# Kernel tuning notes

Measured on AMD Instinct MI355X. Metric: run time of the kernel, lower is better.

The kernel has to match this reference:

```python
import jax, jax.numpy as jnp
import numpy as np

N_NODES = 10000
N_EDGES = 160000
N_TYPES = 128          # rows in SymbolicEmbeddingsVQ table
N_SYMBOLS = 64
PATTERN_LEN = 8
SYMBOL_DIM = 16
HIDDEN = PATTERN_LEN * SYMBOL_DIM  # mode='concat' -> 128
NUM_RADIAL = 6


def setup_inputs() -> dict:
    key = jax.random.key(0)
    ks = jax.random.split(key, 10)
    x = jax.random.randint(ks[0], (N_NODES,), 0, N_TYPES)
    rbf = jax.random.normal(ks[1], (N_EDGES, NUM_RADIAL), dtype=jnp.float32)
    i = jax.random.randint(ks[2], (N_EDGES,), 0, N_NODES)
    j = jax.random.randint(ks[3], (N_EDGES,), 0, N_NODES)
    # VQ symbolic embedding params: each of 128 types is a pattern of
    # PATTERN_LEN symbol ids; symbols are vectors from a codebook.
    code_idx = jax.random.randint(ks[4], (N_TYPES, PATTERN_LEN), 0, N_SYMBOLS)
    codebook = jax.random.normal(ks[5], (N_SYMBOLS, SYMBOL_DIM), dtype=jnp.float32)
    # Linear layers (PyTorch Linear default uniform init approximated by scaled normals)
    W_rbf = jax.random.normal(ks[6], (NUM_RADIAL, HIDDEN), dtype=jnp.float32) / np.sqrt(NUM_RADIAL)
    b_rbf = jnp.zeros((HIDDEN,), dtype=jnp.float32)
    W = jax.random.normal(ks[7], (3 * HIDDEN, HIDDEN), dtype=jnp.float32) / np.sqrt(3 * HIDDEN)
    b = jnp.zeros((HIDDEN,), dtype=jnp.float32)
    return {"x": x, "rbf": rbf, "i": i, "j": j, "code_idx": code_idx,
            "codebook": codebook, "W_rbf": W_rbf, "b_rbf": b_rbf, "W": W, "b": b}


def reference(x, rbf, i, j, code_idx, codebook, W_rbf, b_rbf, W, b):
    act = jax.nn.silu
    # Symbolic VQ embedding, mode='concat': table[t] = concat of PATTERN_LEN codebook vectors
    table = codebook[code_idx].reshape(N_TYPES, HIDDEN)   # [128, hidden]
    h = table[x]                                          # [N_nodes, hidden]
    r = act(rbf @ W_rbf + b_rbf)                          # [E, hidden]
    feat = jnp.concatenate([h[i], h[j], r], axis=-1)      # [E, 3*hidden]
    return act(feat @ W + b)                              # [E, hidden]
```

## Files before the change

### kernel.cpp

```cpp
#include <hip/hip_runtime.h>
#include <hip/hip_bf16.h>
#include <stdint.h>

typedef __attribute__((ext_vector_type(8))) short bf16x8;
typedef __attribute__((ext_vector_type(4))) float f32x4;

__device__ __forceinline__ float silu_f(float x) {
    return x * __builtin_amdgcn_rcpf(1.0f + __expf(-x));
}

__device__ __forceinline__ unsigned short f2bf(float x) {
    union { float f; unsigned int u; } v; v.f = x;
    unsigned int r = v.u + 0x7fffu + ((v.u >> 16) & 1u);
    return (unsigned short)(r >> 16);
}
__device__ __forceinline__ float bf2f(unsigned short u) {
    union { unsigned int u; float f; } v; v.u = ((unsigned int)u) << 16;
    return v.f;
}

__device__ __forceinline__ void async16(void* l, const void* g) {
    auto lds3 = (__attribute__((address_space(3))) unsigned int*)(uintptr_t)l;
    auto g1   = (const __attribute__((address_space(1))) unsigned int*)(uintptr_t)g;
    __builtin_amdgcn_global_load_lds(g1, lds3, 16, 0, 0);
}

__global__ void prep_P(const int* __restrict__ code_idx,
                       const float* __restrict__ codebook,
                       const float* __restrict__ W,
                       const float* __restrict__ b,
                       unsigned short* __restrict__ P1,
                       unsigned short* __restrict__ P2,
                       unsigned short* __restrict__ Wt3)
{
    __shared__ float trow[128];
    const int t = blockIdx.x, tid = threadIdx.x;
    if (tid < 128) {
        int sym = code_idx[t * 8 + (tid >> 4)];
        trow[tid] = codebook[sym * 16 + (tid & 15)];
    } else {
        int k = tid - 128;
        Wt3[t * 128 + k] = f2bf(W[(256 + k) * 128 + t]);
    }
    __syncthreads();
    const int which = tid >> 7, o = tid & 127;
    const float* Wb = W + which * 16384;
    float acc = which ? 0.0f : b[o];
#pragma unroll 8
    for (int k = 0; k < 128; ++k)
        acc += trow[k] * Wb[k * 128 + o];
    (which ? P2 : P1)[t * 128 + o] = f2bf(acc);
}

__global__ __launch_bounds__(256, 3) void fused_main(
    const int* __restrict__ x,
    const float* __restrict__ rbf,
    const int* __restrict__ ei,
    const int* __restrict__ ej,
    const float* __restrict__ W_rbf,
    const float* __restrict__ b_rbf,
    const unsigned short* __restrict__ P1,
    const unsigned short* __restrict__ P2,
    const unsigned short* __restrict__ Wt3,
    float* __restrict__ out)
{
    __shared__ __align__(16) unsigned char lB[32768];
    __shared__ __align__(16) unsigned char lA[16384];
    __shared__ __align__(16) unsigned char lR[1536];

    const int tid  = threadIdx.x;
    const int lane = tid & 63;
    const int w    = tid >> 6;
    const int e0   = blockIdx.x * 64;

    const int quad = lane >> 4, l15 = lane & 15;
    const int wm = (w >> 1) * 32, wn = (w & 1) * 64;

    {
        const int ri = lane >> 4, ch = lane & 15;
#pragma unroll
        for (int rr = 0; rr < 8; ++rr) {
            int g = w * 8 + rr;
            int o = g * 4 + ri;
            int j = ch ^ (o & 7);
            async16(lB + g * 1024, Wt3 + o * 128 + j * 8);
        }
    }
    if (w == 0)
        async16(lR, (const unsigned char*)rbf + (size_t)e0 * 24 + lane * 16);
    else if (w == 1 && lane < 32)
        async16(lR + 1024, (const unsigned char*)rbf + (size_t)e0 * 24 + 1024 + lane * 16);

    int ti[8], tj[8];
#pragma unroll
    for (int mi = 0; mi < 2; ++mi)
#pragma unroll
        for (int r = 0; r < 4; ++r) {
            int m = wm + mi * 16 + quad * 4 + r;
            int e = e0 + m;
            ti[mi * 4 + r] = x[ei[e]];
            tj[mi * 4 + r] = x[ej[e]];
        }

    const int j16 = tid & 15, gg = tid >> 4, cb = j16 * 8;
    float wr[6][8], br[8];
#pragma unroll
    for (int q = 0; q < 6; ++q) {
        const float4* p = (const float4*)(W_rbf + q * 128 + cb);
        float4 a = p[0], c = p[1];
        wr[q][0]=a.x; wr[q][1]=a.y; wr[q][2]=a.z; wr[q][3]=a.w;
        wr[q][4]=c.x; wr[q][5]=c.y; wr[q][6]=c.z; wr[q][7]=c.w;
    }
    {
        const float4* p = (const float4*)(b_rbf + cb);
        float4 a = p[0], c = p[1];
        br[0]=a.x; br[1]=a.y; br[2]=a.z; br[3]=a.w;
        br[4]=c.x; br[5]=c.y; br[6]=c.z; br[7]=c.w;
    }

    __syncthreads();

#pragma unroll
    for (int i = 0; i < 4; ++i) {
        int m = gg * 4 + i;
        const float* rr_ = (const float*)(lR + m * 24);
        float f0 = rr_[0], f1 = rr_[1], f2 = rr_[2],
              f3 = rr_[3], f4 = rr_[4], f5 = rr_[5];
        bf16x8 pk;
#pragma unroll
        for (int c = 0; c < 8; ++c) {
            float a = br[c] + f0*wr[0][c] + f1*wr[1][c] + f2*wr[2][c]
                            + f3*wr[3][c] + f4*wr[4][c] + f5*wr[5][c];
            pk[c] = (short)f2bf(silu_f(a));
        }
        int p = j16 ^ (m & 7);
        *(bf16x8*)(lA + m * 256 + p * 16) = pk;
    }

    __syncthreads();

    unsigned short q1[2][4][4], q2[2][4][4];
#pragma unroll
    for (int mi = 0; mi < 2; ++mi)
#pragma unroll
        for (int r = 0; r < 4; ++r) {
            const unsigned short* p1r = P1 + ti[mi * 4 + r] * 128;
            const unsigned short* p2r = P2 + tj[mi * 4 + r] * 128;
#pragma unroll
            for (int ni = 0; ni < 4; ++ni) {
                int o = wn + ni * 16 + l15;
                q1[mi][r][ni] = p1r[o];
                q2[mi][r][ni] = p2r[o];
            }
        }

    f32x4 acc[2][4] = {};
    const int l7 = l15 & 7;
#pragma unroll
    for (int ks = 0; ks < 4; ++ks) {
        const int j = ks * 4 + quad;
        const int p = j ^ l7;
        bf16x8 af[2], bfv[4];
#pragma unroll
        for (int mi = 0; mi < 2; ++mi)
            af[mi] = *(const bf16x8*)(lA + (wm + mi * 16 + l15) * 256 + p * 16);
#pragma unroll
        for (int ni = 0; ni < 4; ++ni)
            bfv[ni] = *(const bf16x8*)(lB + (wn + ni * 16 + l15) * 256 + p * 16);
#pragma unroll
        for (int mi = 0; mi < 2; ++mi)
#pragma unroll
            for (int ni = 0; ni < 4; ++ni)
                acc[mi][ni] = __builtin_amdgcn_mfma_f32_16x16x32_bf16(
                    af[mi], bfv[ni], acc[mi][ni], 0, 0, 0);
    }

#pragma unroll
    for (int mi = 0; mi < 2; ++mi)
#pragma unroll
        for (int r = 0; r < 4; ++r) {
            int m = wm + mi * 16 + quad * 4 + r;
            size_t e = e0 + m;
#pragma unroll
            for (int ni = 0; ni < 4; ++ni) {
                int o = wn + ni * 16 + l15;
                float v = acc[mi][ni][r] + bf2f(q1[mi][r][ni]) + bf2f(q2[mi][r][ni]);
                out[e * 128 + o] = silu_f(v);
            }
        }
}

extern "C" void kernel_launch(void* const* d_in, const int* in_sizes, int n_in,
                              void* d_out, int out_size, void* d_ws, size_t ws_size,
                              hipStream_t stream) {
    const int*   x        = (const int*)d_in[0];
    const float* rbf      = (const float*)d_in[1];
    const int*   ei       = (const int*)d_in[2];
    const int*   ej       = (const int*)d_in[3];
    const int*   code_idx = (const int*)d_in[4];
    const float* codebook = (const float*)d_in[5];
    const float* W_rbf    = (const float*)d_in[6];
    const float* b_rbf    = (const float*)d_in[7];
    const float* W        = (const float*)d_in[8];
    const float* b        = (const float*)d_in[9];
    float* out = (float*)d_out;

    const int nE = in_sizes[2];

    if (ws_size < 98304) return;
    unsigned short* P1  = (unsigned short*)d_ws;
    unsigned short* P2  = P1 + 16384;
    unsigned short* Wt3 = P2 + 16384;

    prep_P<<<128, 256, 0, stream>>>(code_idx, codebook, W, b, P1, P2, Wt3);
    fused_main<<<nE / 64, 256, 0, stream>>>(x, rbf, ei, ej, W_rbf, b_rbf,
                                            P1, P2, Wt3, out);
}
```

Measured before the change: 132.9 us.

## Make fused kernel persistent with atomic tile queue and double-buffered prefetch

```diff
diff --git a/kernel.cpp b/kernel.cpp
--- a/kernel.cpp
+++ b/kernel.cpp
@@ -3,6 +3,7 @@
 #include <stdint.h>
 
 typedef __attribute__((ext_vector_type(8))) short bf16x8;
+typedef __attribute__((ext_vector_type(4))) short bf16x4;
 typedef __attribute__((ext_vector_type(4))) float f32x4;
 
 __device__ __forceinline__ float silu_f(float x) {
@@ -31,10 +32,12 @@
                        const float* __restrict__ b,
                        unsigned short* __restrict__ P1,
                        unsigned short* __restrict__ P2,
-                       unsigned short* __restrict__ Wt3)
+                       unsigned short* __restrict__ Wt3,
+                       int* __restrict__ counter)
 {
     __shared__ float trow[128];
     const int t = blockIdx.x, tid = threadIdx.x;
+    if (t == 0 && tid == 0) counter[0] = 0;
     if (tid < 128) {
         int sym = code_idx[t * 8 + (tid >> 4)];
         trow[tid] = codebook[sym * 16 + (tid & 15)];
@@ -62,19 +65,22 @@
     const unsigned short* __restrict__ P1,
     const unsigned short* __restrict__ P2,
     const unsigned short* __restrict__ Wt3,
-    float* __restrict__ out)
+    float* __restrict__ out,
+    int* __restrict__ counter,
+    int ntiles)
 {
     __shared__ __align__(16) unsigned char lB[32768];
     __shared__ __align__(16) unsigned char lA[16384];
-    __shared__ __align__(16) unsigned char lR[1536];
+    __shared__ __align__(16) unsigned char lR[2][1536];
+    __shared__ int lTi[2][64], lTj[2][64];
+    __shared__ int lT[2];
 
     const int tid  = threadIdx.x;
     const int lane = tid & 63;
     const int w    = tid >> 6;
-    const int e0   = blockIdx.x * 64;
-
-    const int quad = lane >> 4, l15 = lane & 15;
+    const int quad = lane >> 4, l15 = lane & 15, l7 = lane & 7;
     const int wm = (w >> 1) * 32, wn = (w & 1) * 64;
+    const unsigned char* rbfB = (const unsigned char*)rbf;
 
     {
         const int ri = lane >> 4, ch = lane & 15;
@@ -86,108 +92,131 @@
             async16(lB + g * 1024, Wt3 + o * 128 + j * 8);
         }
     }
+    const int j32 = tid & 31, grp = tid >> 5;
+    const int cb4 = j32 * 4;
+    float wr[6][4], br[4];
+#pragma unroll
+    for (int q = 0; q < 6; ++q) {
+        float4 a = *(const float4*)(W_rbf + q * 128 + cb4);
+        wr[q][0] = a.x; wr[q][1] = a.y; wr[q][2] = a.z; wr[q][3] = a.w;
+    }
+    {
+        float4 a = *(const float4*)(b_rbf + cb4);
+        br[0] = a.x; br[1] = a.y; br[2] = a.z; br[3] = a.w;
+    }
+
+    if (tid == 0) lT[0] = atomicAdd(counter, 1);
+    __syncthreads();
+    int t = lT[0];
+    if (t >= ntiles) return;
+
     if (w == 0)
-        async16(lR, (const unsigned char*)rbf + (size_t)e0 * 24 + lane * 16);
-    else if (w == 1 && lane < 32)
-        async16(lR + 1024, (const unsigned char*)rbf + (size_t)e0 * 24 + 1024 + lane * 16);
-
-    int ti[8], tj[8];
-#pragma unroll
-    for (int mi = 0; mi < 2; ++mi)
-#pragma unroll
-        for (int r = 0; r < 4; ++r) {
-            int m = wm + mi * 16 + quad * 4 + r;
-            int e = e0 + m;
-            ti[mi * 4 + r] = x[ei[e]];
-            tj[mi * 4 + r] = x[ej[e]];
-        }
-
-    const int j16 = tid & 15, gg = tid >> 4, cb = j16 * 8;
-    float wr[6][8], br[8];
-#pragma unroll
-    for (int q = 0; q < 6; ++q) {
-        const float4* p = (const float4*)(W_rbf + q * 128 + cb);
-        float4 a = p[0], c = p[1];
-        wr[q][0]=a.x; wr[q][1]=a.y; wr[q][2]=a.z; wr[q][3]=a.w;
-        wr[q][4]=c.x; wr[q][5]=c.y; wr[q][6]=c.z; wr[q][7]=c.w;
-    }
-    {
-        const float4* p = (const float4*)(b_rbf + cb);
-        float4 a = p[0], c = p[1];
-        br[0]=a.x; br[1]=a.y; br[2]=a.z; br[3]=a.w;
-        br[4]=c.x; br[5]=c.y; br[6]=c.z; br[7]=c.w;
-    }
-
+        async16(lR[0], rbfB + (size_t)t * 1536 + lane * 16);
+    else if (w == 1) {
+        if (lane < 32)
+            async16(lR[0] + 1024, rbfB + (size_t)t * 1536 + 1024 + lane * 16);
+    } else if (w == 2)
+        lTi[0][lane] = x[ei[t * 64 + lane]];
+    else
+        lTj[0][lane] = x[ej[t * 64 + lane]];
+    if (tid == 0) lT[1] = atomicAdd(counter, 1);
     __syncthreads();
 
-#pragma unroll
-    for (int i = 0; i < 4; ++i) {
-        int m = gg * 4 + i;
-        const float* rr_ = (const float*)(lR + m * 24);
-        float f0 = rr_[0], f1 = rr_[1], f2 = rr_[2],
-              f3 = rr_[3], f4 = rr_[4], f5 = rr_[5];
-        bf16x8 pk;
-#pragma unroll
-        for (int c = 0; c < 8; ++c) {
-            float a = br[c] + f0*wr[0][c] + f1*wr[1][c] + f2*wr[2][c]
-                            + f3*wr[3][c] + f4*wr[4][c] + f5*wr[5][c];
-            pk[c] = (short)f2bf(silu_f(a));
-        }
-        int p = j16 ^ (m & 7);
-        *(bf16x8*)(lA + m * 256 + p * 16) = pk;
-    }
-
-    __syncthreads();
-
-    unsigned short q1[2][4][4], q2[2][4][4];
-#pragma unroll
-    for (int mi = 0; mi < 2; ++mi)
-#pragma unroll
-        for (int r = 0; r < 4; ++r) {
-            const unsigned short* p1r = P1 + ti[mi * 4 + r] * 128;
-            const unsigned short* p2r = P2 + tj[mi * 4 + r] * 128;
-#pragma unroll
-            for (int ni = 0; ni < 4; ++ni) {
-                int o = wn + ni * 16 + l15;
-                q1[mi][r][ni] = p1r[o];
-                q2[mi][r][ni] = p2r[o];
+    int cb = 0;
+    for (;;) {
+        const int nb = cb ^ 1;
+        const int t2 = lT[nb];
+        const bool have2 = (t2 < ntiles);
+
+        if (have2) {
+            if (w == 0)
+                async16(lR[nb], rbfB + (size_t)t2 * 1536 + lane * 16);
+            else if (w == 1) {
+                if (lane < 32)
+                    async16(lR[nb] + 1024, rbfB + (size_t)t2 * 1536 + 1024 + lane * 16);
+            } else if (w == 2)
+                lTi[nb][lane] = x[ei[t2 * 64 + lane]];
+            else
+                lTj[nb][lane] = x[ej[t2 * 64 + lane]];
+            if (tid == 0) lT[cb] = atomicAdd(counter, 1);
+        }
+
+#pragma unroll
+        for (int i = 0; i < 8; ++i) {
+            int m = grp * 8 + i;
+            const unsigned char* rp = lR[cb] + m * 24;
+            float2 f01 = *(const float2*)(rp);
+            float2 f23 = *(const float2*)(rp + 8);
+            float2 f45 = *(const float2*)(rp + 16);
+            bf16x4 pk;
+#pragma unroll
+            for (int c = 0; c < 4; ++c) {
+                float a = br[c] + f01.x * wr[0][c] + f01.y * wr[1][c]
+                                + f23.x * wr[2][c] + f23.y * wr[3][c]
+                                + f45.x * wr[4][c] + f45.y * wr[5][c];
+                pk[c] = (short)f2bf(silu_f(a));
             }
-        }
-
-    f32x4 acc[2][4] = {};
-    const int l7 = l15 & 7;
-#pragma unroll
-    for (int ks = 0; ks < 4; ++ks) {
-        const int j = ks * 4 + quad;
-        const int p = j ^ l7;
-        bf16x8 af[2], bfv[4];
+            int p = (j32 >> 1) ^ (m & 7);
+            *(bf16x4*)(lA + m * 256 + p * 16 + (j32 & 1) * 8) = pk;
+        }
+
+        __syncthreads();
+
+        unsigned short q1[2][4][4], q2[2][4][4];
 #pragma unroll
         for (int mi = 0; mi < 2; ++mi)
-            af[mi] = *(const bf16x8*)(lA + (wm + mi * 16 + l15) * 256 + p * 16);
-#pragma unroll
-        for (int ni = 0; ni < 4; ++ni)
-            bfv[ni] = *(const bf16x8*)(lB + (wn + ni * 16 + l15) * 256 + p * 16);
+#pragma unroll
+            for (int r = 0; r < 4; ++r) {
+                int m = wm + mi * 16 + quad * 4 + r;
+                const unsigned short* p1r = P1 + lTi[cb][m] * 128;
+                const unsigned short* p2r = P2 + lTj[cb][m] * 128;
+#pragma unroll
+                for (int ni = 0; ni < 4; ++ni) {
+                    int o = wn + ni * 16 + l15;
+                    q1[mi][r][ni] = p1r[o];
+                    q2[mi][r][ni] = p2r[o];
+                }
+            }
+
+        f32x4 acc[2][4] = {};
+#pragma unroll
+        for (int ks = 0; ks < 4; ++ks) {
+            const int j = ks * 4 + quad;
+            const int p = j ^ l7;
+            bf16x8 af[2], bfv[4];
+#pragma unroll
+            for (int mi = 0; mi < 2; ++mi)
+                af[mi] = *(const bf16x8*)(lA + (wm + mi * 16 + l15) * 256 + p * 16);
+#pragma unroll
+            for (int ni = 0; ni < 4; ++ni)
+                bfv[ni] = *(const bf16x8*)(lB + (wn + ni * 16 + l15) * 256 + p * 16);
+#pragma unroll
+            for (int mi = 0; mi < 2; ++mi)
+#pragma unroll
+                for (int ni = 0; ni < 4; ++ni)
+                    acc[mi][ni] = __builtin_amdgcn_mfma_f32_16x16x32_bf16(
+                        af[mi], bfv[ni], acc[mi][ni], 0, 0, 0);
+        }
+
 #pragma unroll
         for (int mi = 0; mi < 2; ++mi)
 #pragma unroll
-            for (int ni = 0; ni < 4; ++ni)
-                acc[mi][ni] = __builtin_amdgcn_mfma_f32_16x16x32_bf16(
-                    af[mi], bfv[ni], acc[mi][ni], 0, 0, 0);
-    }
-
-#pragma unroll
-    for (int mi = 0; mi < 2; ++mi)
-#pragma unroll
-        for (int r = 0; r < 4; ++r) {
-            int m = wm + mi * 16 + quad * 4 + r;
-            size_t e = e0 + m;
-#pragma unroll
-            for (int ni = 0; ni < 4; ++ni) {
-                int o = wn + ni * 16 + l15;
-                float v = acc[mi][ni][r] + bf2f(q1[mi][r][ni]) + bf2f(q2[mi][r][ni]);
-                out[e * 128 + o] = silu_f(v);
+            for (int r = 0; r < 4; ++r) {
+                int m = wm + mi * 16 + quad * 4 + r;
+                size_t e = (size_t)t * 64 + m;
+#pragma unroll
+                for (int ni = 0; ni < 4; ++ni) {
+                    int o = wn + ni * 16 + l15;
+                    float v = acc[mi][ni][r] + bf2f(q1[mi][r][ni]) + bf2f(q2[mi][r][ni]);
+                    out[e * 128 + o] = silu_f(v);
+                }
             }
-        }
+
+        if (!have2) return;
+        __syncthreads();
+        t = t2;
+        cb = nb;
+    }
 }
 
 extern "C" void kernel_launch(void* const* d_in, const int* in_sizes, int n_in,
@@ -206,13 +235,15 @@
     float* out = (float*)d_out;
 
     const int nE = in_sizes[2];
-
-    if (ws_size < 98304) return;
+    const int ntiles = nE / 64;
+
+    if (ws_size < 98312) return;
     unsigned short* P1  = (unsigned short*)d_ws;
     unsigned short* P2  = P1 + 16384;
     unsigned short* Wt3 = P2 + 16384;
-
-    prep_P<<<128, 256, 0, stream>>>(code_idx, codebook, W, b, P1, P2, Wt3);
-    fused_main<<<nE / 64, 256, 0, stream>>>(x, rbf, ei, ej, W_rbf, b_rbf,
-                                            P1, P2, Wt3, out);
-}
+    int* counter = (int*)((unsigned char*)d_ws + 98304);
+
+    prep_P<<<128, 256, 0, stream>>>(code_idx, codebook, W, b, P1, P2, Wt3, counter);
+    fused_main<<<768, 256, 0, stream>>>(x, rbf, ei, ej, W_rbf, b_rbf,
+                                        P1, P2, Wt3, out, counter, ntiles);
+}
```

After: 155.3 us. +16.8%, slower.

## Compute rbf MLP A-fragments directly in registers and drop the LDS A tile

Applied to the files above, without the earlier changes.

```diff
diff --git a/kernel.cpp b/kernel.cpp
--- a/kernel.cpp
+++ b/kernel.cpp
@@ -52,7 +52,7 @@
     (which ? P2 : P1)[t * 128 + o] = f2bf(acc);
 }
 
-__global__ __launch_bounds__(256, 3) void fused_main(
+__global__ __launch_bounds__(256, 4) void fused_main(
     const int* __restrict__ x,
     const float* __restrict__ rbf,
     const int* __restrict__ ei,
@@ -65,16 +65,16 @@
     float* __restrict__ out)
 {
     __shared__ __align__(16) unsigned char lB[32768];
-    __shared__ __align__(16) unsigned char lA[16384];
-    __shared__ __align__(16) unsigned char lR[1536];
+    __shared__ __align__(16) float lW[6 * 128];
+    __shared__ __align__(16) float lb[128];
+    __shared__ int lTi[64], lTj[64];
 
     const int tid  = threadIdx.x;
     const int lane = tid & 63;
     const int w    = tid >> 6;
-    const int e0   = blockIdx.x * 64;
-
-    const int quad = lane >> 4, l15 = lane & 15;
+    const int quad = lane >> 4, l15 = lane & 15, l7 = lane & 7;
     const int wm = (w >> 1) * 32, wn = (w & 1) * 64;
+    const int e0 = blockIdx.x * 64;
 
     {
         const int ri = lane >> 4, ch = lane & 15;
@@ -86,66 +86,71 @@
             async16(lB + g * 1024, Wt3 + o * 128 + j * 8);
         }
     }
-    if (w == 0)
-        async16(lR, (const unsigned char*)rbf + (size_t)e0 * 24 + lane * 16);
-    else if (w == 1 && lane < 32)
-        async16(lR + 1024, (const unsigned char*)rbf + (size_t)e0 * 24 + 1024 + lane * 16);
-
-    int ti[8], tj[8];
+    if (w == 0) {
+#pragma unroll
+        for (int rr = 0; rr < 3; ++rr)
+            async16((unsigned char*)lW + rr * 1024,
+                    (const unsigned char*)W_rbf + rr * 1024 + lane * 16);
+    } else if (w == 1) {
+        if (lane < 32)
+            async16(lb, (const unsigned char*)b_rbf + lane * 16);
+    } else if (w == 2) {
+        lTi[lane] = x[ei[e0 + lane]];
+    } else {
+        lTj[lane] = x[ej[e0 + lane]];
+    }
+
+    float rb[2][6];
+#pragma unroll
+    for (int mi = 0; mi < 2; ++mi) {
+        const float2* rp = (const float2*)(rbf + (size_t)(e0 + wm + mi * 16 + l15) * 6);
+        float2 a = rp[0], c = rp[1], d = rp[2];
+        rb[mi][0] = a.x; rb[mi][1] = a.y; rb[mi][2] = c.x;
+        rb[mi][3] = c.y; rb[mi][4] = d.x; rb[mi][5] = d.y;
+    }
+
+    __syncthreads();
+
+    bf16x8 afrag[2][4];
+#pragma unroll
+    for (int ks = 0; ks < 4; ++ks) {
+        const int c0 = quad * 8 + 32 * ks;
+        float wq[6][8], bq[8];
+#pragma unroll
+        for (int q = 0; q < 6; ++q) {
+            float4 a = *(const float4*)(lW + q * 128 + c0);
+            float4 c = *(const float4*)(lW + q * 128 + c0 + 4);
+            wq[q][0]=a.x; wq[q][1]=a.y; wq[q][2]=a.z; wq[q][3]=a.w;
+            wq[q][4]=c.x; wq[q][5]=c.y; wq[q][6]=c.z; wq[q][7]=c.w;
+        }
+        {
+            float4 a = *(const float4*)(lb + c0);
+            float4 c = *(const float4*)(lb + c0 + 4);
+            bq[0]=a.x; bq[1]=a.y; bq[2]=a.z; bq[3]=a.w;
+            bq[4]=c.x; bq[5]=c.y; bq[6]=c.z; bq[7]=c.w;
+        }
+#pragma unroll
+        for (int mi = 0; mi < 2; ++mi) {
+            bf16x8 pk;
+#pragma unroll
+            for (int c = 0; c < 8; ++c) {
+                float a = bq[c] + rb[mi][0]*wq[0][c] + rb[mi][1]*wq[1][c]
+                                + rb[mi][2]*wq[2][c] + rb[mi][3]*wq[3][c]
+                                + rb[mi][4]*wq[4][c] + rb[mi][5]*wq[5][c];
+                pk[c] = (short)f2bf(silu_f(a));
+            }
+            afrag[mi][ks] = pk;
+        }
+    }
+
+    unsigned short q1[2][4][4], q2[2][4][4];
 #pragma unroll
     for (int mi = 0; mi < 2; ++mi)
 #pragma unroll
         for (int r = 0; r < 4; ++r) {
             int m = wm + mi * 16 + quad * 4 + r;
-            int e = e0 + m;
-            ti[mi * 4 + r] = x[ei[e]];
-            tj[mi * 4 + r] = x[ej[e]];
-        }
-
-    const int j16 = tid & 15, gg = tid >> 4, cb = j16 * 8;
-    float wr[6][8], br[8];
-#pragma unroll
-    for (int q = 0; q < 6; ++q) {
-        const float4* p = (const float4*)(W_rbf + q * 128 + cb);
-        float4 a = p[0], c = p[1];
-        wr[q][0]=a.x; wr[q][1]=a.y; wr[q][2]=a.z; wr[q][3]=a.w;
-        wr[q][4]=c.x; wr[q][5]=c.y; wr[q][6]=c.z; wr[q][7]=c.w;
-    }
-    {
-        const float4* p = (const float4*)(b_rbf + cb);
-        float4 a = p[0], c = p[1];
-        br[0]=a.x; br[1]=a.y; br[2]=a.z; br[3]=a.w;
-        br[4]=c.x; br[5]=c.y; br[6]=c.z; br[7]=c.w;
-    }
-
-    __syncthreads();
-
-#pragma unroll
-    for (int i = 0; i < 4; ++i) {
-        int m = gg * 4 + i;
-        const float* rr_ = (const float*)(lR + m * 24);
-        float f0 = rr_[0], f1 = rr_[1], f2 = rr_[2],
-              f3 = rr_[3], f4 = rr_[4], f5 = rr_[5];
-        bf16x8 pk;
-#pragma unroll
-        for (int c = 0; c < 8; ++c) {
-            float a = br[c] + f0*wr[0][c] + f1*wr[1][c] + f2*wr[2][c]
-                            + f3*wr[3][c] + f4*wr[4][c] + f5*wr[5][c];
-            pk[c] = (short)f2bf(silu_f(a));
-        }
-        int p = j16 ^ (m & 7);
-        *(bf16x8*)(lA + m * 256 + p * 16) = pk;
-    }
-
-    __syncthreads();
-
-    unsigned short q1[2][4][4], q2[2][4][4];
-#pragma unroll
-    for (int mi = 0; mi < 2; ++mi)
-#pragma unroll
-        for (int r = 0; r < 4; ++r) {
-            const unsigned short* p1r = P1 + ti[mi * 4 + r] * 128;
-            const unsigned short* p2r = P2 + tj[mi * 4 + r] * 128;
+            const unsigned short* p1r = P1 + lTi[m] * 128;
+            const unsigned short* p2r = P2 + lTj[m] * 128;
 #pragma unroll
             for (int ni = 0; ni < 4; ++ni) {
                 int o = wn + ni * 16 + l15;
@@ -155,15 +160,11 @@
         }
 
     f32x4 acc[2][4] = {};
-    const int l7 = l15 & 7;
 #pragma unroll
     for (int ks = 0; ks < 4; ++ks) {
         const int j = ks * 4 + quad;
         const int p = j ^ l7;
-        bf16x8 af[2], bfv[4];
-#pragma unroll
-        for (int mi = 0; mi < 2; ++mi)
-            af[mi] = *(const bf16x8*)(lA + (wm + mi * 16 + l15) * 256 + p * 16);
+        bf16x8 bfv[4];
 #pragma unroll
         for (int ni = 0; ni < 4; ++ni)
             bfv[ni] = *(const bf16x8*)(lB + (wn + ni * 16 + l15) * 256 + p * 16);
@@ -172,7 +173,7 @@
 #pragma unroll
             for (int ni = 0; ni < 4; ++ni)
                 acc[mi][ni] = __builtin_amdgcn_mfma_f32_16x16x32_bf16(
-                    af[mi], bfv[ni], acc[mi][ni], 0, 0, 0);
+                    afrag[mi][ks], bfv[ni], acc[mi][ni], 0, 0, 0);
     }
 
 #pragma unroll
@@ -180,7 +181,7 @@
 #pragma unroll
         for (int r = 0; r < 4; ++r) {
             int m = wm + mi * 16 + quad * 4 + r;
-            size_t e = e0 + m;
+            size_t e = (size_t)e0 + m;
 #pragma unroll
             for (int ni = 0; ni < 4; ++ni) {
                 int o = wn + ni * 16 + l15;
```

New measurement: 136.7 us. 2.8% more time.
